# Kernel tuning notes

Hardware: AMD Instinct MI355X
Metric: run time of the kernel (lower is better)

The kernel has to match this reference:

```python
import jax, jax.numpy as jnp
import numpy as np

NEG = -1e30  # stands in for -inf on the diagonal; exp(NEG - max) == 0 exactly


def setup_inputs() -> dict:
    key = jax.random.key(0)
    k1, k2, k3, k4, k5 = jax.random.split(key, 5)
    B, C, H, W = 4, 512, 128, 128
    mid = C // 8  # 64
    x = jax.random.normal(k1, (B, C, H, W), dtype=jnp.float32)
    Wq = jax.random.normal(k2, (mid, C), dtype=jnp.float32) * (1.0 / np.sqrt(C))
    Wk = jax.random.normal(k3, (mid, C), dtype=jnp.float32) * (1.0 / np.sqrt(C))
    Wv = jax.random.normal(k4, (C, C), dtype=jnp.float32) * (1.0 / np.sqrt(C))
    gamma = jax.random.normal(k5, (1,), dtype=jnp.float32) * 0.1
    return {"x": x, "Wq": Wq, "Wk": Wk, "Wv": Wv, "gamma": gamma}


def reference(x, Wq, Wk, Wv, gamma):
    B, C, H, W = x.shape
    # 1x1 convs == channel matmuls
    q = jnp.einsum('bchw,mc->bmhw', x, Wq)  # (B, mid, H, W)
    k = jnp.einsum('bchw,mc->bmhw', x, Wk)
    v = jnp.einsum('bchw,dc->bdhw', x, Wv)  # (B, C, H, W)

    # vertical (H-axis) logits with -inf diagonal: eH[b,i,w,j] = sum_m q[b,m,i,w] k[b,m,j,w]
    eH = jnp.einsum('bmiw,bmjw->biwj', q, k)           # (B, H, W, H)
    diag = jnp.eye(H, dtype=bool)[:, None, :]          # (H, 1, H)
    eH = jnp.where(diag, NEG, eH)

    # horizontal (W-axis) logits: eW[b,h,i,j] = sum_m q[b,m,h,i] k[b,m,h,j]
    eW = jnp.einsum('bmhi,bmhj->bhij', q, k)           # (B, H, W, W)

    # joint softmax over the concatenated H+W logits
    attn = jax.nn.softmax(jnp.concatenate([eH, eW], axis=3), axis=3)  # (B, H, W, H+W)
    aH = attn[:, :, :, :H]  # (B, H, W, H)
    aW = attn[:, :, :, H:]  # (B, H, W, W)

    # attention-weighted value aggregation along each axis
    outH = jnp.einsum('bcjw,biwj->bciw', v, aH)  # (B, C, H, W)
    outW = jnp.einsum('bchj,bhij->bchi', v, aW)  # (B, C, H, W)

    return gamma[0] * (outH + outW) + x
```

## Files before the change

### kernel.cpp

```cpp
#include <hip/hip_runtime.h>
#include <cstdint>
#include <cstddef>

#define NEGV (-1e30f)

constexpr int C_ = 512, H_ = 128, W_ = 128;
constexpr int P_ = 16384;

typedef short bf16x8 __attribute__((ext_vector_type(8)));
typedef float f32x4  __attribute__((ext_vector_type(4)));
#define MFMA16(a, b, c) __builtin_amdgcn_mfma_f32_16x16x32_bf16((a), (b), (c), 0, 0, 0)

#define SWZ128(r, cs) (((r) << 7) + (((((cs) >> 3) ^ ((r) & 7))) << 3) + ((cs) & 7))
#define SWZ64(r, cs)  (((r) << 6) + (((((cs) >> 3) ^ ((r) & 7))) << 3) + ((cs) & 7))

__device__ inline void gl_lds16(const void* g, void* l) {
    __builtin_amdgcn_global_load_lds(
        (const __attribute__((address_space(1))) unsigned int*)g,
        (__attribute__((address_space(3))) unsigned int*)l, 16, 0, 0);
}

__device__ inline unsigned short f2bf(float f) {
    union { float f; uint32_t i; } t; t.f = f;
    uint32_t r = t.i + 0x7FFFu + ((t.i >> 16) & 1u);
    return (unsigned short)(r >> 16);
}

__global__ __launch_bounds__(256) void kwconv(
    const float* __restrict__ Wq, const float* __restrict__ Wk,
    const float* __restrict__ Wv,
    unsigned short* __restrict__ Wqkbf, unsigned short* __restrict__ Wvbf)
{
    const int i4 = (blockIdx.x * 256 + threadIdx.x) * 4;
    const float* src; unsigned short* dst; int off;
    if (i4 < 32768)       { src = Wq + i4;          dst = Wqkbf + i4; }
    else if (i4 < 65536)  { off = i4 - 32768; src = Wk + off; dst = Wqkbf + i4; }
    else                  { off = i4 - 65536; src = Wv + off; dst = Wvbf + off; }
    const float4 v = *(const float4*)src;
    ushort4 u; u.x = f2bf(v.x); u.y = f2bf(v.y); u.z = f2bf(v.z); u.w = f2bf(v.w);
    *(ushort4*)dst = u;
}

__global__ __launch_bounds__(256) void kprep1(
    const float* __restrict__ x, unsigned short* __restrict__ xTbf)
{
    __shared__ float t[32][33];
    const int tx = threadIdx.x, ty = threadIdx.y;
    const int h0 = (blockIdx.x >> 2) * 32, w0 = (blockIdx.x & 3) * 32;
    const size_t base = (size_t)blockIdx.y * P_;
#pragma unroll
    for (int k = 0; k < 4; k++)
        t[ty + 8 * k][tx] = x[base + (size_t)(h0 + ty + 8 * k) * 128 + w0 + tx];
    __syncthreads();
#pragma unroll
    for (int k = 0; k < 4; k++)
        xTbf[base + (size_t)(w0 + ty + 8 * k) * 128 + h0 + tx] = f2bf(t[tx][ty + 8 * k]);
}

__global__ __launch_bounds__(256) void kprep2(
    const float* __restrict__ x, unsigned short* __restrict__ xbfT)
{
    __shared__ float t[32][33];
    const int tx = threadIdx.x, ty = threadIdx.y;
    const int p0 = blockIdx.x * 32, c0 = blockIdx.y * 32, b = blockIdx.z;
#pragma unroll
    for (int k = 0; k < 4; k++)
        t[ty + 8 * k][tx] = x[((size_t)(b * C_ + c0 + ty + 8 * k)) * P_ + p0 + tx];
    __syncthreads();
#pragma unroll
    for (int k = 0; k < 4; k++)
        xbfT[((size_t)b * P_ + p0 + ty + 8 * k) * C_ + c0 + tx] = f2bf(t[tx][ty + 8 * k]);
}

__global__ __launch_bounds__(256) void kgemmqk(
    const unsigned short* __restrict__ A, const unsigned short* __restrict__ Bm,
    unsigned short* __restrict__ outbf)
{
    __shared__ __attribute__((aligned(16))) unsigned short sA[128 * 72];
    __shared__ __attribute__((aligned(16))) unsigned short sB[128 * 72];
    const int tid = threadIdx.x;
    const int pbase = blockIdx.x * 128, b = blockIdx.z;
    const int lane = tid & 63, wv = tid >> 6;
    const int m0 = (wv >> 1) * 64, p0 = (wv & 1) * 64;
    const int fr = lane & 15, fq = lane >> 4;

    f32x4 acc[4][4];
#pragma unroll
    for (int i = 0; i < 4; i++)
#pragma unroll
        for (int j = 0; j < 4; j++) acc[i][j] = (f32x4){0.f, 0.f, 0.f, 0.f};

    const size_t brow0 = ((size_t)b * P_ + pbase) * 512;

    for (int kc = 0; kc < 512; kc += 64) {
#pragma unroll
        for (int rep = 0; rep < 4; rep++) {
            const int idx = rep * 256 + tid;
            const int kg = idx & 7, r = idx >> 3;
            *(uint4*)&sA[r * 72 + kg * 8] = *(const uint4*)&A[(size_t)r * 512 + kc + kg * 8];
            *(uint4*)&sB[r * 72 + kg * 8] = *(const uint4*)&Bm[brow0 + (size_t)r * 512 + kc + kg * 8];
        }
        __syncthreads();
#pragma unroll
        for (int kk = 0; kk < 64; kk += 32) {
            bf16x8 af[4], bfv[4];
#pragma unroll
            for (int t = 0; t < 4; t++) af[t]  = *(const bf16x8*)&sA[(m0 + t * 16 + fr) * 72 + kk + fq * 8];
#pragma unroll
            for (int t = 0; t < 4; t++) bfv[t] = *(const bf16x8*)&sB[(p0 + t * 16 + fr) * 72 + kk + fq * 8];
#pragma unroll
            for (int i = 0; i < 4; i++)
#pragma unroll
                for (int j = 0; j < 4; j++)
                    acc[i][j] = MFMA16(af[i], bfv[j], acc[i][j]);
        }
        __syncthreads();
    }

#pragma unroll
    for (int tj = 0; tj < 4; tj++) {
        const int p_g = pbase + p0 + tj * 16 + fr;
        const size_t rowo = ((size_t)b * P_ + p_g) * 128;
#pragma unroll
        for (int ti = 0; ti < 4; ti++) {
            const int mk = m0 + ti * 16 + fq * 4;
            ushort4 u;
            u.x = f2bf(acc[ti][tj][0]); u.y = f2bf(acc[ti][tj][1]);
            u.z = f2bf(acc[ti][tj][2]); u.w = f2bf(acc[ti][tj][3]);
            *(ushort4*)&outbf[rowo + mk] = u;
        }
    }
}

__global__ __launch_bounds__(256) void klogits(
    const unsigned short* __restrict__ qkP,
    float* __restrict__ ERow, float* __restrict__ ECol)
{
    __shared__ __attribute__((aligned(16))) unsigned short sPM[128 * 136];
    const int tid = threadIdx.x;
    const int s = blockIdx.x, b = blockIdx.y, mode = blockIdx.z;
    const int rowMul  = mode ? 1 : 128;
    const int rowStep = mode ? 128 : 1;
    float* E = mode ? ECol : ERow;
    const size_t qbase = (size_t)b * P_ * 128;
    const int rb = s * rowMul;
#pragma unroll
    for (int rep = 0; rep < 8; rep++) {
        const int idx = rep * 256 + tid;
        const int mkg = idx & 15, i = idx >> 4;
        *(uint4*)&sPM[i * 136 + mkg * 8] =
            *(const uint4*)&qkP[qbase + (size_t)(rb + i * rowStep) * 128 + mkg * 8];
    }
    __syncthreads();

    const int lane = tid & 63, wv = tid >> 6;
    const int i0 = (wv >> 1) * 64, j0 = (wv & 1) * 64;
    const int fr = lane & 15, fq = lane >> 4;

    f32x4 acc[4][4];
#pragma unroll
    for (int i = 0; i < 4; i++)
#pragma unroll
        for (int j = 0; j < 4; j++) acc[i][j] = (f32x4){0.f, 0.f, 0.f, 0.f};

#pragma unroll
    for (int kk = 0; kk < 64; kk += 32) {
        bf16x8 af[4], bfv[4];
#pragma unroll
        for (int t = 0; t < 4; t++) af[t]  = *(const bf16x8*)&sPM[(i0 + t * 16 + fr) * 136 + kk + fq * 8];
#pragma unroll
        for (int t = 0; t < 4; t++) bfv[t] = *(const bf16x8*)&sPM[(j0 + t * 16 + fr) * 136 + 64 + kk + fq * 8];
#pragma unroll
        for (int i = 0; i < 4; i++)
#pragma unroll
            for (int j = 0; j < 4; j++)
                acc[i][j] = MFMA16(af[i], bfv[j], acc[i][j]);
    }

    float* Eb = E + ((size_t)(b * 128 + s)) * P_;
#pragma unroll
    for (int ti = 0; ti < 4; ti++)
#pragma unroll
        for (int r = 0; r < 4; r++) {
            const int i_g = i0 + ti * 16 + fq * 4 + r;
#pragma unroll
            for (int tj = 0; tj < 4; tj++) {
                const int j_g = j0 + tj * 16 + fr;
                float v = acc[ti][tj][r];
                if (mode && i_g == j_g) v = NEGV;
                Eb[(size_t)i_g * 128 + j_g] = v;
            }
        }
}

__global__ __launch_bounds__(256) void ksoftmax(
    const float* __restrict__ ER, const float* __restrict__ EC,
    unsigned short* __restrict__ AR, unsigned short* __restrict__ AC)
{
    const int lane = threadIdx.x & 63;
    const int pix = blockIdx.x * 4 + (threadIdx.x >> 6);
    const int b = pix >> 14, rem = pix & 16383;
    const int h = rem >> 7, w = rem & 127;
    const size_t ro = ((size_t)((b * 128 + h) * 128 + w)) * 128;
    const size_t co = ((size_t)((b * 128 + w) * 128 + h)) * 128;
    const float2 r = *(const float2*)(ER + ro + lane * 2);
    const float2 c = *(const float2*)(EC + co + lane * 2);
    float mx = fmaxf(fmaxf(r.x, r.y), fmaxf(c.x, c.y));
#pragma unroll
    for (int off = 32; off > 0; off >>= 1) mx = fmaxf(mx, __shfl_xor(mx, off));
    const float e0 = __expf(r.x - mx), e1 = __expf(r.y - mx);
    const float e2 = __expf(c.x - mx), e3 = __expf(c.y - mx);
    float sm = e0 + e1 + e2 + e3;
#pragma unroll
    for (int off = 32; off > 0; off >>= 1) sm += __shfl_xor(sm, off);
    const float inv = 1.0f / sm;
    ushort2 u0; u0.x = f2bf(e0 * inv); u0.y = f2bf(e1 * inv);
    ushort2 u1; u1.x = f2bf(e2 * inv); u1.y = f2bf(e3 * inv);
    *(ushort2*)(AR + ro + lane * 2) = u0;
    *(ushort2*)(AC + co + lane * 2) = u1;
}

__global__ __launch_bounds__(256) void kagg2(
    const unsigned short* __restrict__ ARow, const unsigned short* __restrict__ ACol,
    const float* __restrict__ x, const unsigned short* __restrict__ xTbf,
    unsigned short* __restrict__ ySumR, unsigned short* __restrict__ ySumC)
{
    __shared__ __attribute__((aligned(16))) unsigned short sAttn[128 * 128];
    __shared__ __attribute__((aligned(16))) unsigned short sX[128 * 128];
    const int tid = threadIdx.x;
    const int s = blockIdx.x, b = blockIdx.y, mode = blockIdx.z;
    const int lane = tid & 63, wv = tid >> 6;
    const int m0 = (wv >> 1) * 64, n0 = (wv & 1) * 64;
    const int fr = lane & 15, fq = lane >> 4;

    const unsigned short* At = (mode ? ACol : ARow) + ((size_t)(b * 128 + s)) * P_;
#pragma unroll
    for (int rep = 0; rep < 8; rep++) {
        const int idx = rep * 256 + tid;
        const int r = idx >> 4, sl = idx & 15;
        gl_lds16(&At[(size_t)r * 128 + (sl ^ (r & 7)) * 8], &sAttn[idx * 8]);
    }

    unsigned short* yS = mode ? ySumC : ySumR;

    for (int ct = 0; ct < 4; ct++) {
        if (mode == 0) {
            const float* Xf = &x[((size_t)(b * C_ + ct * 128)) * P_ + s * 128];
#pragma unroll
            for (int rep = 0; rep < 16; rep++) {
                const int idx = rep * 256 + tid;
                const int jq = idx & 31, cc = idx >> 5;
                const float4 v = *(const float4*)&Xf[(size_t)cc * P_ + jq * 4];
                ushort4 u; u.x = f2bf(v.x); u.y = f2bf(v.y); u.z = f2bf(v.z); u.w = f2bf(v.w);
                *(ushort4*)&sX[SWZ128(cc, jq * 4)] = u;
            }
        } else {
            const unsigned short* Xs = &xTbf[((size_t)(b * C_ + ct * 128)) * P_ + s * 128];
#pragma unroll
            for (int rep = 0; rep < 8; rep++) {
                const int idx = rep * 256 + tid;
                const int r = idx >> 4, sl = idx & 15;
                gl_lds16(&Xs[(size_t)r * P_ + (sl ^ (r & 7)) * 8], &sX[idx * 8]);
            }
        }
        __syncthreads();

        f32x4 acc[4][4];
#pragma unroll
        for (int i = 0; i < 4; i++)
#pragma unroll
            for (int j = 0; j < 4; j++) acc[i][j] = (f32x4){0.f, 0.f, 0.f, 0.f};

#pragma unroll
        for (int kk = 0; kk < 128; kk += 32) {
            bf16x8 af[4], bfv[4];
#pragma unroll
            for (int t = 0; t < 4; t++) {
                const int rc = m0 + t * 16 + fr;
                af[t] = *(const bf16x8*)&sX[SWZ128(rc, kk + fq * 8)];
            }
#pragma unroll
            for (int t = 0; t < 4; t++) {
                const int ri = n0 + t * 16 + fr;
                bfv[t] = *(const bf16x8*)&sAttn[SWZ128(ri, kk + fq * 8)];
            }
#pragma unroll
            for (int i = 0; i < 4; i++)
#pragma unroll
                for (int j = 0; j < 4; j++)
                    acc[i][j] = MFMA16(af[i], bfv[j], acc[i][j]);
        }

        const int cg0 = ct * 128 + m0 + fq * 4;
#pragma unroll
        for (int tj = 0; tj < 4; tj++) {
            const int i_g = n0 + tj * 16 + fr;
            const size_t p = mode ? ((size_t)i_g * 128 + s) : ((size_t)s * 128 + i_g);
            unsigned short* rowp = yS + ((size_t)b * P_ + p) * 512;
#pragma unroll
            for (int ti = 0; ti < 4; ti++) {
                ushort4 u;
                u.x = f2bf(acc[ti][tj][0]); u.y = f2bf(acc[ti][tj][1]);
                u.z = f2bf(acc[ti][tj][2]); u.w = f2bf(acc[ti][tj][3]);
                *(ushort4*)&rowp[cg0 + ti * 16] = u;
            }
        }
        __syncthreads();
    }
}

__global__ __launch_bounds__(256) void kfinal(
    const unsigned short* __restrict__ Wvbf,
    const unsigned short* __restrict__ yR,
    const unsigned short* __restrict__ yC,
    float* __restrict__ outf,
    const float* __restrict__ addx,
    const float* __restrict__ gammap)
{
    __shared__ __attribute__((aligned(16))) unsigned short sM[128 * 64];
    __shared__ __attribute__((aligned(16))) unsigned short sP[128 * 64];
    const int tid = threadIdx.x;
    const int pbase = blockIdx.x * 128, mt = blockIdx.y, b = blockIdx.z;
    const int lane = tid & 63, wv = tid >> 6;
    const int p0 = (wv >> 1) * 64, m0 = (wv & 1) * 64;
    const int fr = lane & 15, fq = lane >> 4;

    f32x4 acc[4][4];
#pragma unroll
    for (int i = 0; i < 4; i++)
#pragma unroll
        for (int j = 0; j < 4; j++) acc[i][j] = (f32x4){0.f, 0.f, 0.f, 0.f};

    const unsigned short* Arow = Wvbf + (size_t)(mt * 128) * 512;
    const size_t brow = ((size_t)b * P_ + pbase) * 512;

    for (int chunk = 0; chunk < 16; ++chunk) {
        const int kc = (chunk & 7) * 64;
        const unsigned short* Bp = (chunk < 8 ? yR : yC) + brow + kc;
        const unsigned short* Ap = Arow + kc;
        if (chunk) __syncthreads();
#pragma unroll
        for (int rep = 0; rep < 4; rep++) {
            const int idx = rep * 256 + tid;
            const int r = idx >> 3, kgs = (idx & 7) ^ (r & 7);
            gl_lds16(&Ap[(size_t)r * 512 + kgs * 8], &sM[idx * 8]);
            gl_lds16(&Bp[(size_t)r * 512 + kgs * 8], &sP[idx * 8]);
        }
        __syncthreads();
#pragma unroll
        for (int kk = 0; kk < 64; kk += 32) {
            bf16x8 ap[4], am[4];
#pragma unroll
            for (int t = 0; t < 4; t++) {
                const int rp = p0 + t * 16 + fr;
                ap[t] = *(const bf16x8*)&sP[SWZ64(rp, kk + fq * 8)];
            }
#pragma unroll
            for (int t = 0; t < 4; t++) {
                const int rm = m0 + t * 16 + fr;
                am[t] = *(const bf16x8*)&sM[SWZ64(rm, kk + fq * 8)];
            }
#pragma unroll
            for (int i = 0; i < 4; i++)
#pragma unroll
                for (int j = 0; j < 4; j++)
                    acc[i][j] = MFMA16(ap[i], am[j], acc[i][j]);
        }
    }

    const float g = gammap[0];
#pragma unroll
    for (int ti = 0; ti < 4; ti++) {
        const int p_g = pbase + p0 + ti * 16 + fq * 4;
#pragma unroll
        for (int tj = 0; tj < 4; tj++) {
            const int m_g = mt * 128 + m0 + tj * 16 + fr;
            const size_t off = ((size_t)(b * 512 + m_g)) * P_ + p_g;
            const float4 xa = *(const float4*)&addx[off];
            float4 o;
            o.x = fmaf(g, acc[ti][tj][0], xa.x);
            o.y = fmaf(g, acc[ti][tj][1], xa.y);
            o.z = fmaf(g, acc[ti][tj][2], xa.z);
            o.w = fmaf(g, acc[ti][tj][3], xa.w);
            *(float4*)&outf[off] = o;
        }
    }
}

extern "C" void kernel_launch(void* const* d_in, const int* in_sizes, int n_in,
                              void* d_out, int out_size, void* d_ws, size_t ws_size,
                              hipStream_t stream) {
    const float* x     = (const float*)d_in[0];
    const float* Wq    = (const float*)d_in[1];
    const float* Wk    = (const float*)d_in[2];
    const float* Wv    = (const float*)d_in[3];
    const float* gamma = (const float*)d_in[4];
    float* out = (float*)d_out;

    char* base = (char*)d_ws;
    unsigned short* Wqkbf = (unsigned short*)base;             base += 131072;
    unsigned short* Wvbf  = (unsigned short*)base;             base += 524288;
    unsigned short* xTbf  = (unsigned short*)base;             base += 67108864;
    unsigned short* xbfT  = (unsigned short*)base;             base += 67108864;
    unsigned short* qkP   = (unsigned short*)base;             base += 16777216;
    float*          ERow  = (float*)base;                      base += 33554432;
    float*          ECol  = (float*)base;                      base += 33554432;
    unsigned short* ARow  = (unsigned short*)base;             base += 16777216;
    unsigned short* ACol  = (unsigned short*)base;             base += 16777216;
    unsigned short* ySumR = (unsigned short*)base;             base += 67108864;
    unsigned short* ySumC = (unsigned short*)ERow;

    kwconv<<<320, 256, 0, stream>>>(Wq, Wk, Wv, Wqkbf, Wvbf);
    kprep1<<<dim3(16, 2048), dim3(32, 8), 0, stream>>>(x, xTbf);
    kprep2<<<dim3(512, 16, 4), dim3(32, 8), 0, stream>>>(x, xbfT);
    kgemmqk<<<dim3(128, 1, 4), 256, 0, stream>>>(Wqkbf, xbfT, qkP);
    klogits<<<dim3(128, 4, 2), 256, 0, stream>>>(qkP, ERow, ECol);
    ksoftmax<<<16384, 256, 0, stream>>>(ERow, ECol, ARow, ACol);
    kagg2<<<dim3(128, 4, 2), 256, 0, stream>>>(ARow, ACol, x, xTbf, ySumR, ySumC);
    kfinal<<<dim3(128, 4, 4), 256, 0, stream>>>(Wvbf, ySumR, ySumC, out, x, gamma);
}
```

Baseline: 537.6 us.

## Store logits as fp16, double-buffer GEMM loads, vectorize transpose kernels

```diff
diff --git a/kernel.cpp b/kernel.cpp
--- a/kernel.cpp
+++ b/kernel.cpp
@@ -9,6 +9,7 @@
 
 typedef short bf16x8 __attribute__((ext_vector_type(8)));
 typedef float f32x4  __attribute__((ext_vector_type(4)));
+typedef _Float16 f16x4 __attribute__((ext_vector_type(4)));
 #define MFMA16(a, b, c) __builtin_amdgcn_mfma_f32_16x16x32_bf16((a), (b), (c), 0, 0, 0)
 
 #define SWZ128(r, cs) (((r) << 7) + (((((cs) >> 3) ^ ((r) & 7))) << 3) + ((cs) & 7))
@@ -45,39 +46,51 @@
     const float* __restrict__ x, unsigned short* __restrict__ xTbf)
 {
     __shared__ float t[32][33];
-    const int tx = threadIdx.x, ty = threadIdx.y;
+    const int tid = threadIdx.x;
     const int h0 = (blockIdx.x >> 2) * 32, w0 = (blockIdx.x & 3) * 32;
     const size_t base = (size_t)blockIdx.y * P_;
-#pragma unroll
-    for (int k = 0; k < 4; k++)
-        t[ty + 8 * k][tx] = x[base + (size_t)(h0 + ty + 8 * k) * 128 + w0 + tx];
+    {
+        const int r = tid >> 3, c4 = (tid & 7) * 4;
+        const float4 v = *(const float4*)&x[base + (size_t)(h0 + r) * 128 + w0 + c4];
+        t[r][c4] = v.x; t[r][c4 + 1] = v.y; t[r][c4 + 2] = v.z; t[r][c4 + 3] = v.w;
+    }
     __syncthreads();
-#pragma unroll
-    for (int k = 0; k < 4; k++)
-        xTbf[base + (size_t)(w0 + ty + 8 * k) * 128 + h0 + tx] = f2bf(t[tx][ty + 8 * k]);
+    {
+        const int wr = tid >> 3, hc = (tid & 7) * 4;
+        ushort4 u;
+        u.x = f2bf(t[hc][wr]);     u.y = f2bf(t[hc + 1][wr]);
+        u.z = f2bf(t[hc + 2][wr]); u.w = f2bf(t[hc + 3][wr]);
+        *(ushort4*)&xTbf[base + (size_t)(w0 + wr) * 128 + h0 + hc] = u;
+    }
 }
 
 __global__ __launch_bounds__(256) void kprep2(
     const float* __restrict__ x, unsigned short* __restrict__ xbfT)
 {
     __shared__ float t[32][33];
-    const int tx = threadIdx.x, ty = threadIdx.y;
+    const int tid = threadIdx.x;
     const int p0 = blockIdx.x * 32, c0 = blockIdx.y * 32, b = blockIdx.z;
-#pragma unroll
-    for (int k = 0; k < 4; k++)
-        t[ty + 8 * k][tx] = x[((size_t)(b * C_ + c0 + ty + 8 * k)) * P_ + p0 + tx];
+    {
+        const int r = tid >> 3, c4 = (tid & 7) * 4;
+        const float4 v = *(const float4*)&x[((size_t)(b * C_ + c0 + r)) * P_ + p0 + c4];
+        t[r][c4] = v.x; t[r][c4 + 1] = v.y; t[r][c4 + 2] = v.z; t[r][c4 + 3] = v.w;
+    }
     __syncthreads();
-#pragma unroll
-    for (int k = 0; k < 4; k++)
-        xbfT[((size_t)b * P_ + p0 + ty + 8 * k) * C_ + c0 + tx] = f2bf(t[tx][ty + 8 * k]);
+    {
+        const int pr = tid >> 3, cc = (tid & 7) * 4;
+        ushort4 u;
+        u.x = f2bf(t[cc][pr]);     u.y = f2bf(t[cc + 1][pr]);
+        u.z = f2bf(t[cc + 2][pr]); u.w = f2bf(t[cc + 3][pr]);
+        *(ushort4*)&xbfT[((size_t)b * P_ + p0 + pr) * C_ + c0 + cc] = u;
+    }
 }
 
 __global__ __launch_bounds__(256) void kgemmqk(
     const unsigned short* __restrict__ A, const unsigned short* __restrict__ Bm,
     unsigned short* __restrict__ outbf)
 {
-    __shared__ __attribute__((aligned(16))) unsigned short sA[128 * 72];
-    __shared__ __attribute__((aligned(16))) unsigned short sB[128 * 72];
+    __shared__ __attribute__((aligned(16))) unsigned short sA[2][128 * 64];
+    __shared__ __attribute__((aligned(16))) unsigned short sB[2][128 * 64];
     const int tid = threadIdx.x;
     const int pbase = blockIdx.x * 128, b = blockIdx.z;
     const int lane = tid & 63, wv = tid >> 6;
@@ -92,30 +105,43 @@
 
     const size_t brow0 = ((size_t)b * P_ + pbase) * 512;
 
-    for (int kc = 0; kc < 512; kc += 64) {
-#pragma unroll
-        for (int rep = 0; rep < 4; rep++) {
-            const int idx = rep * 256 + tid;
-            const int kg = idx & 7, r = idx >> 3;
-            *(uint4*)&sA[r * 72 + kg * 8] = *(const uint4*)&A[(size_t)r * 512 + kc + kg * 8];
-            *(uint4*)&sB[r * 72 + kg * 8] = *(const uint4*)&Bm[brow0 + (size_t)r * 512 + kc + kg * 8];
-        }
-        __syncthreads();
+#define QK_STAGE(chunk, buf) {                                                  \
+        const int kc_ = (chunk) * 64;                                           \
+        _Pragma("unroll")                                                       \
+        for (int rep = 0; rep < 4; rep++) {                                     \
+            const int idx = rep * 256 + tid;                                    \
+            const int r_ = idx >> 3, kgs = (idx & 7) ^ (r_ & 7);                \
+            gl_lds16(&A[(size_t)r_ * 512 + kc_ + kgs * 8], &sA[buf][idx * 8]);  \
+            gl_lds16(&Bm[brow0 + (size_t)r_ * 512 + kc_ + kgs * 8], &sB[buf][idx * 8]); \
+        } }
+
+    QK_STAGE(0, 0);
+    int cur = 0;
+    for (int chunk = 0; chunk < 8; ++chunk) {
+        if (chunk < 7) {
+            QK_STAGE(chunk + 1, cur ^ 1);
+            asm volatile("s_waitcnt vmcnt(8)" ::: "memory");
+        } else {
+            asm volatile("s_waitcnt vmcnt(0)" ::: "memory");
+        }
+        __builtin_amdgcn_s_barrier();
 #pragma unroll
         for (int kk = 0; kk < 64; kk += 32) {
             bf16x8 af[4], bfv[4];
 #pragma unroll
-            for (int t = 0; t < 4; t++) af[t]  = *(const bf16x8*)&sA[(m0 + t * 16 + fr) * 72 + kk + fq * 8];
-#pragma unroll
-            for (int t = 0; t < 4; t++) bfv[t] = *(const bf16x8*)&sB[(p0 + t * 16 + fr) * 72 + kk + fq * 8];
+            for (int t = 0; t < 4; t++) af[t]  = *(const bf16x8*)&sA[cur][SWZ64(m0 + t * 16 + fr, kk + fq * 8)];
+#pragma unroll
+            for (int t = 0; t < 4; t++) bfv[t] = *(const bf16x8*)&sB[cur][SWZ64(p0 + t * 16 + fr, kk + fq * 8)];
 #pragma unroll
             for (int i = 0; i < 4; i++)
 #pragma unroll
                 for (int j = 0; j < 4; j++)
                     acc[i][j] = MFMA16(af[i], bfv[j], acc[i][j]);
         }
-        __syncthreads();
-    }
+        if (chunk < 7) __builtin_amdgcn_s_barrier();
+        cur ^= 1;
+    }
+#undef QK_STAGE
 
 #pragma unroll
     for (int tj = 0; tj < 4; tj++) {
@@ -134,14 +160,14 @@
 
 __global__ __launch_bounds__(256) void klogits(
     const unsigned short* __restrict__ qkP,
-    float* __restrict__ ERow, float* __restrict__ ECol)
+    _Float16* __restrict__ ERow, _Float16* __restrict__ ECol)
 {
     __shared__ __attribute__((aligned(16))) unsigned short sPM[128 * 136];
     const int tid = threadIdx.x;
     const int s = blockIdx.x, b = blockIdx.y, mode = blockIdx.z;
     const int rowMul  = mode ? 1 : 128;
     const int rowStep = mode ? 128 : 1;
-    float* E = mode ? ECol : ERow;
+    _Float16* E = mode ? ECol : ERow;
     const size_t qbase = (size_t)b * P_ * 128;
     const int rb = s * rowMul;
 #pragma unroll
@@ -177,7 +203,7 @@
                 acc[i][j] = MFMA16(af[i], bfv[j], acc[i][j]);
     }
 
-    float* Eb = E + ((size_t)(b * 128 + s)) * P_;
+    _Float16* Eb = E + ((size_t)(b * 128 + s)) * P_;
 #pragma unroll
     for (int ti = 0; ti < 4; ti++)
 #pragma unroll
@@ -187,37 +213,44 @@
             for (int tj = 0; tj < 4; tj++) {
                 const int j_g = j0 + tj * 16 + fr;
                 float v = acc[ti][tj][r];
-                if (mode && i_g == j_g) v = NEGV;
-                Eb[(size_t)i_g * 128 + j_g] = v;
+                if (mode && i_g == j_g) v = -60000.0f;
+                Eb[(size_t)i_g * 128 + j_g] = (_Float16)v;
             }
         }
 }
 
 __global__ __launch_bounds__(256) void ksoftmax(
-    const float* __restrict__ ER, const float* __restrict__ EC,
+    const _Float16* __restrict__ ER, const _Float16* __restrict__ EC,
     unsigned short* __restrict__ AR, unsigned short* __restrict__ AC)
 {
-    const int lane = threadIdx.x & 63;
-    const int pix = blockIdx.x * 4 + (threadIdx.x >> 6);
+    const int tid = threadIdx.x;
+    const int l32 = tid & 31;
+    const int pix = blockIdx.x * 8 + (tid >> 5);
     const int b = pix >> 14, rem = pix & 16383;
     const int h = rem >> 7, w = rem & 127;
     const size_t ro = ((size_t)((b * 128 + h) * 128 + w)) * 128;
     const size_t co = ((size_t)((b * 128 + w) * 128 + h)) * 128;
-    const float2 r = *(const float2*)(ER + ro + lane * 2);
-    const float2 c = *(const float2*)(EC + co + lane * 2);
-    float mx = fmaxf(fmaxf(r.x, r.y), fmaxf(c.x, c.y));
-#pragma unroll
-    for (int off = 32; off > 0; off >>= 1) mx = fmaxf(mx, __shfl_xor(mx, off));
-    const float e0 = __expf(r.x - mx), e1 = __expf(r.y - mx);
-    const float e2 = __expf(c.x - mx), e3 = __expf(c.y - mx);
-    float sm = e0 + e1 + e2 + e3;
-#pragma unroll
-    for (int off = 32; off > 0; off >>= 1) sm += __shfl_xor(sm, off);
+    const f16x4 r = *(const f16x4*)(ER + ro + l32 * 4);
+    const f16x4 c = *(const f16x4*)(EC + co + l32 * 4);
+    const float r0 = r.x, r1 = r.y, r2 = r.z, r3 = r.w;
+    const float c0 = c.x, c1 = c.y, c2 = c.z, c3 = c.w;
+    float mx = fmaxf(fmaxf(fmaxf(r0, r1), fmaxf(r2, r3)),
+                     fmaxf(fmaxf(c0, c1), fmaxf(c2, c3)));
+#pragma unroll
+    for (int off = 16; off > 0; off >>= 1) mx = fmaxf(mx, __shfl_xor(mx, off));
+    const float e0 = __expf(r0 - mx), e1 = __expf(r1 - mx);
+    const float e2 = __expf(r2 - mx), e3 = __expf(r3 - mx);
+    const float f0 = __expf(c0 - mx), f1 = __expf(c1 - mx);
+    const float f2 = __expf(c2 - mx), f3 = __expf(c3 - mx);
+    float sm = (e0 + e1 + e2 + e3) + (f0 + f1 + f2 + f3);
+#pragma unroll
+    for (int off = 16; off > 0; off >>= 1) sm += __shfl_xor(sm, off);
     const float inv = 1.0f / sm;
-    ushort2 u0; u0.x = f2bf(e0 * inv); u0.y = f2bf(e1 * inv);
-    ushort2 u1; u1.x = f2bf(e2 * inv); u1.y = f2bf(e3 * inv);
-    *(ushort2*)(AR + ro + lane * 2) = u0;
-    *(ushort2*)(AC + co + lane * 2) = u1;
+    ushort4 u0, u1;
+    u0.x = f2bf(e0 * inv); u0.y = f2bf(e1 * inv); u0.z = f2bf(e2 * inv); u0.w = f2bf(e3 * inv);
+    u1.x = f2bf(f0 * inv); u1.y = f2bf(f1 * inv); u1.z = f2bf(f2 * inv); u1.w = f2bf(f3 * inv);
+    *(ushort4*)(AR + ro + l32 * 4) = u0;
+    *(ushort4*)(AC + co + l32 * 4) = u1;
 }
 
 __global__ __launch_bounds__(256) void kagg2(
@@ -317,8 +350,8 @@
     const float* __restrict__ addx,
     const float* __restrict__ gammap)
 {
-    __shared__ __attribute__((aligned(16))) unsigned short sM[128 * 64];
-    __shared__ __attribute__((aligned(16))) unsigned short sP[128 * 64];
+    __shared__ __attribute__((aligned(16))) unsigned short sM[2][128 * 64];
+    __shared__ __attribute__((aligned(16))) unsigned short sP[2][128 * 64];
     const int tid = threadIdx.x;
     const int pbase = blockIdx.x * 128, mt = blockIdx.y, b = blockIdx.z;
     const int lane = tid & 63, wv = tid >> 6;
@@ -334,39 +367,45 @@
     const unsigned short* Arow = Wvbf + (size_t)(mt * 128) * 512;
     const size_t brow = ((size_t)b * P_ + pbase) * 512;
 
+#define FIN_STAGE(chunk, buf) {                                                 \
+        const int kc_ = ((chunk) & 7) * 64;                                     \
+        const unsigned short* Bp = ((chunk) < 8 ? yR : yC) + brow + kc_;        \
+        const unsigned short* Ap = Arow + kc_;                                  \
+        _Pragma("unroll")                                                       \
+        for (int rep = 0; rep < 4; rep++) {                                     \
+            const int idx = rep * 256 + tid;                                    \
+            const int r_ = idx >> 3, kgs = (idx & 7) ^ (r_ & 7);                \
+            gl_lds16(&Ap[(size_t)r_ * 512 + kgs * 8], &sM[buf][idx * 8]);       \
+            gl_lds16(&Bp[(size_t)r_ * 512 + kgs * 8], &sP[buf][idx * 8]);       \
+        } }
+
+    FIN_STAGE(0, 0);
+    int cur = 0;
     for (int chunk = 0; chunk < 16; ++chunk) {
-        const int kc = (chunk & 7) * 64;
-        const unsigned short* Bp = (chunk < 8 ? yR : yC) + brow + kc;
-        const unsigned short* Ap = Arow + kc;
-        if (chunk) __syncthreads();
-#pragma unroll
-        for (int rep = 0; rep < 4; rep++) {
-            const int idx = rep * 256 + tid;
-            const int r = idx >> 3, kgs = (idx & 7) ^ (r & 7);
-            gl_lds16(&Ap[(size_t)r * 512 + kgs * 8], &sM[idx * 8]);
-            gl_lds16(&Bp[(size_t)r * 512 + kgs * 8], &sP[idx * 8]);
-        }
-        __syncthreads();
+        if (chunk < 15) {
+            FIN_STAGE(chunk + 1, cur ^ 1);
+            asm volatile("s_waitcnt vmcnt(8)" ::: "memory");
+        } else {
+            asm volatile("s_waitcnt vmcnt(0)" ::: "memory");
+        }
+        __builtin_amdgcn_s_barrier();
 #pragma unroll
         for (int kk = 0; kk < 64; kk += 32) {
             bf16x8 ap[4], am[4];
 #pragma unroll
-            for (int t = 0; t < 4; t++) {
-                const int rp = p0 + t * 16 + fr;
-                ap[t] = *(const bf16x8*)&sP[SWZ64(rp, kk + fq * 8)];
-            }
-#pragma unroll
-            for (int t = 0; t < 4; t++) {
-                const int rm = m0 + t * 16 + fr;
-                am[t] = *(const bf16x8*)&sM[SWZ64(rm, kk + fq * 8)];
-            }
+            for (int t = 0; t < 4; t++) ap[t] = *(const bf16x8*)&sP[cur][SWZ64(p0 + t * 16 + fr, kk + fq * 8)];
+#pragma unroll
+            for (int t = 0; t < 4; t++) am[t] = *(const bf16x8*)&sM[cur][SWZ64(m0 + t * 16 + fr, kk + fq * 8)];
 #pragma unroll
             for (int i = 0; i < 4; i++)
 #pragma unroll
                 for (int j = 0; j < 4; j++)
                     acc[i][j] = MFMA16(ap[i], am[j], acc[i][j]);
         }
-    }
+        if (chunk < 15) __builtin_amdgcn_s_barrier();
+        cur ^= 1;
+    }
+#undef FIN_STAGE
 
     const float g = gammap[0];
 #pragma unroll
@@ -403,19 +442,19 @@
     unsigned short* xTbf  = (unsigned short*)base;             base += 67108864;
     unsigned short* xbfT  = (unsigned short*)base;             base += 67108864;
     unsigned short* qkP   = (unsigned short*)base;             base += 16777216;
-    float*          ERow  = (float*)base;                      base += 33554432;
-    float*          ECol  = (float*)base;                      base += 33554432;
+    _Float16*       ERow  = (_Float16*)base;                   base += 33554432;
+    _Float16*       ECol  = (_Float16*)base;                   base += 33554432;
     unsigned short* ARow  = (unsigned short*)base;             base += 16777216;
     unsigned short* ACol  = (unsigned short*)base;             base += 16777216;
     unsigned short* ySumR = (unsigned short*)base;             base += 67108864;
     unsigned short* ySumC = (unsigned short*)ERow;
 
     kwconv<<<320, 256, 0, stream>>>(Wq, Wk, Wv, Wqkbf, Wvbf);
-    kprep1<<<dim3(16, 2048), dim3(32, 8), 0, stream>>>(x, xTbf);
-    kprep2<<<dim3(512, 16, 4), dim3(32, 8), 0, stream>>>(x, xbfT);
+    kprep1<<<dim3(16, 2048), 256, 0, stream>>>(x, xTbf);
+    kprep2<<<dim3(512, 16, 4), 256, 0, stream>>>(x, xbfT);
     kgemmqk<<<dim3(128, 1, 4), 256, 0, stream>>>(Wqkbf, xbfT, qkP);
     klogits<<<dim3(128, 4, 2), 256, 0, stream>>>(qkP, ERow, ECol);
-    ksoftmax<<<16384, 256, 0, stream>>>(ERow, ECol, ARow, ACol);
+    ksoftmax<<<8192, 256, 0, stream>>>(ERow, ECol, ARow, ACol);
     kagg2<<<dim3(128, 4, 2), 256, 0, stream>>>(ARow, ACol, x, xTbf, ySumR, ySumC);
     kfinal<<<dim3(128, 4, 4), 256, 0, stream>>>(Wvbf, ySumR, ySumC, out, x, gamma);
 }
```

After: 515.6 us. -4.1%, faster.
